# Optimization experiments

Hardware: AMD Instinct MI355X
Metric: run time of the kernel (lower is better)

## Reference

```python
import jax, jax.numpy as jnp
import numpy as np

EPS = 1e-5  # eqx.nn.LayerNorm default


def _layer_norm(x, w, b):
    m = x.mean(-1, keepdims=True)
    v = ((x - m) ** 2).mean(-1, keepdims=True)
    return (x - m) / jnp.sqrt(v + EPS) * w + b


def _s4_block(x, nw, nb, lre, lim, bre, bim, cre, cim, d, lstep, ow, ob, o2w, o2b):
    # x: [L, H]. One SequenceBlock: LayerNorm -> S4 recurrence (lax.scan) -> GELU -> GLU-style gated linear -> residual.
    skip = x
    h = _layer_norm(x, nw, nb)
    Lam = lre + 1j * lim                      # [H, N] complex diagonal state matrix
    step = jnp.exp(lstep)[:, None]            # [H, 1] per-channel timescale
    BL = 1.0 / (1.0 - (step / 2.0) * Lam)     # bilinear discretization
    Abar = BL * (1.0 + (step / 2.0) * Lam)    # [H, N]
    Bbar = BL * step * (bre + 1j * bim)       # [H, N]
    C = cre + 1j * cim                        # [H, N]

    def scan_fn(state, u):                    # state: [H, N] complex, u: [H]
        new = Abar * state + Bbar * u[:, None]
        y = 2.0 * jnp.sum(C * new, axis=-1).real + d * u
        return new, y

    init = jnp.zeros(Abar.shape, Abar.dtype)  # cell.init_state
    _, y = jax.lax.scan(scan_fn, init, h)     # [L, H]
    y = jax.nn.gelu(y)
    y = (y @ ow.T + ob) * jax.nn.sigmoid(y @ o2w.T + o2b)
    return skip + y


def setup_inputs() -> dict:
    key = jax.random.key(0)
    L, IN, OUT, H, N, NL = 2048, 4, 3, 512, 32, 4
    ks = jax.random.split(key, 16)
    return {
        "x": jax.random.normal(ks[0], (L, IN), jnp.float32),
        "enc_w": jax.random.normal(ks[1], (H, IN), jnp.float32) / np.sqrt(IN),
        "enc_b": jnp.zeros((H,), jnp.float32),
        "dec_w": jax.random.normal(ks[2], (OUT, H), jnp.float32) / np.sqrt(H),
        "dec_b": jnp.zeros((OUT,), jnp.float32),
        "norm_w": jnp.ones((NL, H), jnp.float32),
        "norm_b": jnp.zeros((NL, H), jnp.float32),
        "lam_re": -0.5 - jax.random.uniform(ks[3], (NL, H, N), jnp.float32),  # stable (Re < 0)
        "lam_im": np.pi * jax.random.normal(ks[4], (NL, H, N), jnp.float32),
        "b_re": jax.random.normal(ks[5], (NL, H, N), jnp.float32) / np.sqrt(N),
        "b_im": jax.random.normal(ks[6], (NL, H, N), jnp.float32) / np.sqrt(N),
        "c_re": jax.random.normal(ks[7], (NL, H, N), jnp.float32) / np.sqrt(N),
        "c_im": jax.random.normal(ks[8], (NL, H, N), jnp.float32) / np.sqrt(N),
        "d": jax.random.normal(ks[9], (NL, H), jnp.float32),
        "log_step": float(np.log(1e-3)) + float(np.log(1e-1) - np.log(1e-3)) * jax.random.uniform(ks[10], (NL, H), jnp.float32),
        "out_w": jax.random.normal(ks[11], (NL, H, H), jnp.float32) / np.sqrt(H),
        "out_b": jnp.zeros((NL, H), jnp.float32),
        "out2_w": jax.random.normal(ks[12], (NL, H, H), jnp.float32) / np.sqrt(H),
        "out2_b": jnp.zeros((NL, H), jnp.float32),
    }


def reference(x, enc_w, enc_b, dec_w, dec_b, norm_w, norm_b, lam_re, lam_im, b_re, b_im, c_re, c_im, d, log_step, out_w, out_b, out2_w, out2_b):
    h = x @ enc_w.T + enc_b                   # encoder: [L, IN] -> [L, H]
    for i in range(norm_w.shape[0]):          # fixed small n_layers loop
        h = _s4_block(h, norm_w[i], norm_b[i], lam_re[i], lam_im[i], b_re[i], b_im[i],
                      c_re[i], c_im[i], d[i], log_step[i], out_w[i], out_b[i], out2_w[i], out2_b[i])
    return h @ dec_w.T + dec_b                # decoder: [L, H] -> [L, OUT]
```

## Files before the change

kernel.cpp:

```cpp
#include <hip/hip_runtime.h>
#include <hip/hip_bf16.h>
#include <math.h>

#define LSEQ 2048
#define HD   512
#define NST  32
#define LC   32
#define NCHK 64
#define HH   (HD * HD)

typedef __bf16 bf16;
typedef __bf16 bf16x8 __attribute__((ext_vector_type(8)));
typedef float  floatx4 __attribute__((ext_vector_type(4)));

__device__ __forceinline__ float wave_reduce_add(float v) {
#pragma unroll
    for (int m = 32; m; m >>= 1) v += __shfl_xor(v, m, 64);
    return v;
}

__device__ __forceinline__ float gelu_tanh(float x) {
    float z = 0.7978845608028654f * (x + 0.044715f * x * x * x);
    float e = __expf(2.f * z);
    float th = 1.f - 2.f / (e + 1.f);
    return 0.5f * x * (1.f + th);
}

__device__ __forceinline__ void make_ab(float lre, float lim, float step,
                                        float br0, float bi0,
                                        float& ar, float& ai, float& br, float& bi) {
    float s2 = 0.5f * step;
    float dr = 1.f - s2 * lre, di = -s2 * lim;
    float inv = 1.f / (dr * dr + di * di);
    float blr = dr * inv, bli = -di * inv;
    float nr = 1.f + s2 * lre, ni = s2 * lim;
    ar = blr * nr - bli * ni;
    ai = blr * ni + bli * nr;
    float tr = step * br0, ti = step * bi0;
    br = blr * tr - bli * ti;
    bi = blr * ti + bli * tr;
}

__global__ __launch_bounds__(256) void setup_kernel(
    const float* __restrict__ x,   const float* __restrict__ ew,
    const float* __restrict__ eb,
    const float* __restrict__ lre, const float* __restrict__ lim,
    const float* __restrict__ bre, const float* __restrict__ bim,
    const float* __restrict__ cre, const float* __restrict__ cim,
    const float* __restrict__ ls,  const float* __restrict__ ow,
    const float* __restrict__ o2w,
    float* __restrict__ h, bf16* __restrict__ wb,
    float2* __restrict__ cA, float2* __restrict__ cB,
    float2* __restrict__ cC, float2* __restrict__ cAp,
    float* __restrict__ st0)
{
    int bid = blockIdx.x, tid = threadIdx.x;
    if (bid < 256) {
        int tg = bid * 256 + tid;
        int lay = tg >> 14, rem = tg & 16383;
        int ch = rem >> 5, n = rem & 31;
        float step = __expf(ls[lay * HD + ch]);
        float ar, ai, br, bi;
        make_ab(lre[tg], lim[tg], step, bre[tg], bim[tg], ar, ai, br, bi);
        float xr = ar, xi = ai;
#pragma unroll
        for (int q = 0; q < 5; ++q) { float tt = xr * xr - xi * xi; xi = 2.f * xr * xi; xr = tt; }
        int dst = (lay * NST + n) * HD + ch;
        cA[dst]  = make_float2(ar, ai);
        cB[dst]  = make_float2(br, bi);
        cC[dst]  = make_float2(2.f * cre[tg], 2.f * cim[tg]);
        cAp[dst] = make_float2(xr, xi);
    } else if (bid < 768) {
        int i = ((bid - 256) * 256 + tid) * 8;
        float4 a = *(const float4*)(ow + i);
        float4 b = *(const float4*)(ow + i + 4);
        bf16x8 o;
        o[0]=(bf16)a.x; o[1]=(bf16)a.y; o[2]=(bf16)a.z; o[3]=(bf16)a.w;
        o[4]=(bf16)b.x; o[5]=(bf16)b.y; o[6]=(bf16)b.z; o[7]=(bf16)b.w;
        *(bf16x8*)(wb + i) = o;
        a = *(const float4*)(o2w + i);
        b = *(const float4*)(o2w + i + 4);
        o[0]=(bf16)a.x; o[1]=(bf16)a.y; o[2]=(bf16)a.z; o[3]=(bf16)a.w;
        o[4]=(bf16)b.x; o[5]=(bf16)b.y; o[6]=(bf16)b.z; o[7]=(bf16)b.w;
        *(bf16x8*)(wb + 4 * HH + i) = o;
    } else {
        int i = (bid - 768) * 256 + tid;
        int t = i >> 9, c = i & 511;
        float4 xv = *(const float4*)(x + t * 4);
        float4 wv = *(const float4*)(ew + c * 4);
        float acc = eb[c];
        acc = fmaf(xv.x, wv.x, acc); acc = fmaf(xv.y, wv.y, acc);
        acc = fmaf(xv.z, wv.z, acc); acc = fmaf(xv.w, wv.w, acc);
        h[i] = acc;
        float s1 = wave_reduce_add(acc);
        float s2 = wave_reduce_add(acc * acc);
        if ((tid & 63) == 0) {
            atomicAdd(&st0[t * 2],     s1);
            atomicAdd(&st0[t * 2 + 1], s2);
        }
    }
}

__global__ __launch_bounds__(256, 2) void p1_kernel(
    const float* __restrict__ h, const float* __restrict__ st,
    const float2* __restrict__ cA, const float2* __restrict__ cB,
    const float* __restrict__ nw, const float* __restrict__ nb,
    float2* __restrict__ f, int lay) {
    __shared__ float  tile[4 * LC * 16];
    __shared__ float2 sml[128];
    __shared__ float  snw[16], snb[16];
    int tid = threadIdx.x;
    int lane = tid & 63, w = tid >> 6;
    int chl = lane & 15;
    int ch = blockIdx.x * 16 + chl;
    int sub = lane >> 4;
    int chunk = blockIdx.y * 4 + w;
    int t0 = blockIdx.y * 4 * LC;
    const float* ub = h + (size_t)t0 * HD + blockIdx.x * 16;
#pragma unroll
    for (int r = 0; r < 8; ++r) {
        int idx = r * 256 + tid;
        tile[idx] = ub[(idx >> 4) * HD + (idx & 15)];
    }
    if (tid < 128) {
        float s1 = st[(t0 + tid) * 2], s2 = st[(t0 + tid) * 2 + 1];
        float m = s1 * (1.f / HD);
        float var = s2 * (1.f / HD) - m * m;
        sml[tid] = make_float2(m, rsqrtf(var + 1e-5f));
    }
    if (tid < 16) {
        snw[tid] = nw[lay * HD + blockIdx.x * 16 + tid];
        snb[tid] = nb[lay * HD + blockIdx.x * 16 + tid];
    }
    int cbase = (lay * NST + sub * 8) * HD + ch;
    float aR[8], aI[8], bR[8], bI[8];
#pragma unroll
    for (int j = 0; j < 8; ++j) {
        float2 t = cA[cbase + j * HD]; aR[j] = t.x; aI[j] = t.y;
        t = cB[cbase + j * HD];        bR[j] = t.x; bI[j] = t.y;
    }
    float sr[8], si[8];
#pragma unroll
    for (int j = 0; j < 8; ++j) { sr[j] = 0.f; si[j] = 0.f; }
    __syncthreads();
    float wch = snw[chl], bch = snb[chl];
#pragma unroll 4
    for (int t = 0; t < LC; ++t) {
        int row = w * LC + t;
        float2 ms = sml[row];
        float uu = (tile[row * 16 + chl] - ms.x) * ms.y * wch + bch;
#pragma unroll
        for (int j = 0; j < 8; ++j) {
            float nr = fmaf(aR[j], sr[j], fmaf(-aI[j], si[j], bR[j] * uu));
            float ni = fmaf(aI[j], sr[j], fmaf( aR[j], si[j], bI[j] * uu));
            sr[j] = nr; si[j] = ni;
        }
    }
    float2* fp = f + ((size_t)chunk * NST + sub * 8) * HD + ch;
#pragma unroll
    for (int j = 0; j < 8; ++j) fp[j * HD] = make_float2(sr[j], si[j]);
}

__global__ __launch_bounds__(256) void p2_kernel(
    float2* __restrict__ f, const float2* __restrict__ cAp, int lay) {
    int w = threadIdx.x >> 6, lane = threadIdx.x & 63;
    int chain = blockIdx.x * 4 + w;
    int ch = chain & 511, n = chain >> 9;
    float2 ap = cAp[(lay * NST + n) * HD + ch];
    size_t idx = ((size_t)lane * NST + n) * HD + ch;
    float2 v = f[idx];
    float vr = v.x, vi = v.y, wr = ap.x, wi = ap.y;
#pragma unroll
    for (int d = 1; d < 64; d <<= 1) {
        float pvr = __shfl_up(vr, d, 64);
        float pvi = __shfl_up(vi, d, 64);
        float pwr = __shfl_up(wr, d, 64);
        float pwi = __shfl_up(wi, d, 64);
        if (lane >= d) {
            vr += wr * pvr - wi * pvi;
            vi += wr * pvi + wi * pvr;
            float nr = wr * pwr - wi * pwi;
            float ni = wr * pwi + wi * pwr;
            wr = nr; wi = ni;
        }
    }
    f[idx] = make_float2(vr, vi);
}

__global__ __launch_bounds__(256, 2) void p3_kernel(
    const float* __restrict__ h, const float* __restrict__ st,
    const float2* __restrict__ f,
    const float2* __restrict__ cA, const float2* __restrict__ cB,
    const float2* __restrict__ cC, const float* __restrict__ dd,
    const float* __restrict__ nw, const float* __restrict__ nb,
    bf16* __restrict__ g, int lay) {
    __shared__ float  tile[4 * LC * 16];
    __shared__ float2 sml[128];
    __shared__ float  snw[16], snb[16];
    int tid = threadIdx.x;
    int lane = tid & 63, w = tid >> 6;
    int chl = lane & 15;
    int ch = blockIdx.x * 16 + chl;
    int sub = lane >> 4;
    int chunk = blockIdx.y * 4 + w;
    int t0 = blockIdx.y * 4 * LC;
    const float* ub = h + (size_t)t0 * HD + blockIdx.x * 16;
#pragma unroll
    for (int r = 0; r < 8; ++r) {
        int idx = r * 256 + tid;
        tile[idx] = ub[(idx >> 4) * HD + (idx & 15)];
    }
    if (tid < 128) {
        float s1 = st[(t0 + tid) * 2], s2 = st[(t0 + tid) * 2 + 1];
        float m = s1 * (1.f / HD);
        float var = s2 * (1.f / HD) - m * m;
        sml[tid] = make_float2(m, rsqrtf(var + 1e-5f));
    }
    if (tid < 16) {
        snw[tid] = nw[lay * HD + blockIdx.x * 16 + tid];
        snb[tid] = nb[lay * HD + blockIdx.x * 16 + tid];
    }
    int cbase = (lay * NST + sub * 8) * HD + ch;
    float aR[8], aI[8], bR[8], bI[8], cR[8], cI[8];
#pragma unroll
    for (int j = 0; j < 8; ++j) {
        float2 t = cA[cbase + j * HD]; aR[j] = t.x; aI[j] = t.y;
        t = cB[cbase + j * HD];        bR[j] = t.x; bI[j] = t.y;
        t = cC[cbase + j * HD];        cR[j] = t.x; cI[j] = t.y;
    }
    float dch = dd[lay * HD + ch];
    float sr[8], si[8];
    if (chunk > 0) {
        const float2* ip = f + ((size_t)(chunk - 1) * NST + sub * 8) * HD + ch;
#pragma unroll
        for (int j = 0; j < 8; ++j) { float2 v = ip[j * HD]; sr[j] = v.x; si[j] = v.y; }
    } else {
#pragma unroll
        for (int j = 0; j < 8; ++j) { sr[j] = 0.f; si[j] = 0.f; }
    }
    __syncthreads();
    float wch = snw[chl], bch = snb[chl];
    bf16* gp = g + (size_t)chunk * LC * HD + ch;
#pragma unroll 4
    for (int t = 0; t < LC; ++t) {
        int row = w * LC + t;
        float2 ms = sml[row];
        float uu = (tile[row * 16 + chl] - ms.x) * ms.y * wch + bch;
        float p = 0.f;
#pragma unroll
        for (int j = 0; j < 8; ++j) {
            float nr = fmaf(aR[j], sr[j], fmaf(-aI[j], si[j], bR[j] * uu));
            float ni = fmaf(aI[j], sr[j], fmaf( aR[j], si[j], bI[j] * uu));
            sr[j] = nr; si[j] = ni;
            p = fmaf(cR[j], nr, fmaf(-cI[j], ni, p));
        }
        p += __shfl_xor(p, 16);
        p += __shfl_xor(p, 32);
        float y = fmaf(dch, uu, p);
        if (sub == 0) gp[t * HD] = (bf16)gelu_tanh(y);
    }
}

__global__ __launch_bounds__(256) void mm_kernel(
    const bf16* __restrict__ A,
    const bf16* __restrict__ W1,
    const bf16* __restrict__ W2,
    const float* __restrict__ bias1, const float* __restrict__ bias2,
    float* __restrict__ Hio, float* __restrict__ stn) {
    const int w = threadIdx.x >> 6, lane = threadIdx.x & 63;
    const int wm = w >> 1, wn = w & 1;
    const int mBase = blockIdx.y * 64 + wm * 32;
    const int nBase = blockIdx.x * 64 + wn * 32;
    const int lrow = lane & 15, quad = lane >> 4;

    floatx4 acc1[2][2] = {{{0.f,0.f,0.f,0.f},{0.f,0.f,0.f,0.f}},{{0.f,0.f,0.f,0.f},{0.f,0.f,0.f,0.f}}};
    floatx4 acc2[2][2] = {{{0.f,0.f,0.f,0.f},{0.f,0.f,0.f,0.f}},{{0.f,0.f,0.f,0.f},{0.f,0.f,0.f,0.f}}};

    for (int k0 = 0; k0 < HD; k0 += 32) {
        int kk = k0 + quad * 8;
        bf16x8 a0 = *(const bf16x8*)(A + (mBase + lrow) * HD + kk);
        bf16x8 a1 = *(const bf16x8*)(A + (mBase + 16 + lrow) * HD + kk);
        bf16x8 p0 = *(const bf16x8*)(W1 + (nBase + lrow) * HD + kk);
        bf16x8 p1 = *(const bf16x8*)(W1 + (nBase + 16 + lrow) * HD + kk);
        bf16x8 q0 = *(const bf16x8*)(W2 + (nBase + lrow) * HD + kk);
        bf16x8 q1 = *(const bf16x8*)(W2 + (nBase + 16 + lrow) * HD + kk);
        acc1[0][0] = __builtin_amdgcn_mfma_f32_16x16x32_bf16(a0, p0, acc1[0][0], 0, 0, 0);
        acc1[0][1] = __builtin_amdgcn_mfma_f32_16x16x32_bf16(a0, p1, acc1[0][1], 0, 0, 0);
        acc1[1][0] = __builtin_amdgcn_mfma_f32_16x16x32_bf16(a1, p0, acc1[1][0], 0, 0, 0);
        acc1[1][1] = __builtin_amdgcn_mfma_f32_16x16x32_bf16(a1, p1, acc1[1][1], 0, 0, 0);
        acc2[0][0] = __builtin_amdgcn_mfma_f32_16x16x32_bf16(a0, q0, acc2[0][0], 0, 0, 0);
        acc2[0][1] = __builtin_amdgcn_mfma_f32_16x16x32_bf16(a0, q1, acc2[0][1], 0, 0, 0);
        acc2[1][0] = __builtin_amdgcn_mfma_f32_16x16x32_bf16(a1, q0, acc2[1][0], 0, 0, 0);
        acc2[1][1] = __builtin_amdgcn_mfma_f32_16x16x32_bf16(a1, q1, acc2[1][1], 0, 0, 0);
    }

    float hv[2][2][4];
#pragma unroll
    for (int fm = 0; fm < 2; ++fm)
#pragma unroll
        for (int fn = 0; fn < 2; ++fn) {
            int j = nBase + fn * 16 + lrow;
            float bb1 = bias1[j], bb2 = bias2[j];
#pragma unroll
            for (int r = 0; r < 4; ++r) {
                int t = mBase + fm * 16 + quad * 4 + r;
                float z1 = acc1[fm][fn][r] + bb1;
                float z2 = acc2[fm][fn][r] + bb2;
                float nv = Hio[t * HD + j] + z1 / (1.f + __expf(-z2));
                Hio[t * HD + j] = nv;
                hv[fm][fn][r] = nv;
            }
        }
#pragma unroll
    for (int fm = 0; fm < 2; ++fm)
#pragma unroll
        for (int r = 0; r < 4; ++r) {
            int t = mBase + fm * 16 + quad * 4 + r;
            float s1 = hv[fm][0][r] + hv[fm][1][r];
            float s2 = hv[fm][0][r] * hv[fm][0][r] + hv[fm][1][r] * hv[fm][1][r];
#pragma unroll
            for (int m = 1; m < 16; m <<= 1) {
                s1 += __shfl_xor(s1, m);
                s2 += __shfl_xor(s2, m);
            }
            if (lrow == 0) {
                atomicAdd(&stn[t * 2],     s1);
                atomicAdd(&stn[t * 2 + 1], s2);
            }
        }
}

__global__ __launch_bounds__(192) void dec_kernel(
    const float* __restrict__ h, const float* __restrict__ w,
    const float* __restrict__ b, float* __restrict__ out) {
    int j = threadIdx.x >> 6, lane = threadIdx.x & 63;
    int t = blockIdx.x;
    const float* hp = h + t * HD + lane * 8;
    float v[8];
    *(float4*)(v)     = *(const float4*)(hp);
    *(float4*)(v + 4) = *(const float4*)(hp + 4);
    float w8[8];
    *(float4*)(w8)     = *(const float4*)(w + j * HD + lane * 8);
    *(float4*)(w8 + 4) = *(const float4*)(w + j * HD + lane * 8 + 4);
    float s = 0.f;
#pragma unroll
    for (int e = 0; e < 8; ++e) s = fmaf(v[e], w8[e], s);
    s = wave_reduce_add(s);
    if (lane == 0) out[t * 3 + j] = s + b[j];
}

extern "C" void kernel_launch(void* const* d_in, const int* in_sizes, int n_in,
                              void* d_out, int out_size, void* d_ws, size_t ws_size,
                              hipStream_t stream) {
    const float* x   = (const float*)d_in[0];
    const float* ew  = (const float*)d_in[1];
    const float* eb  = (const float*)d_in[2];
    const float* dw  = (const float*)d_in[3];
    const float* db  = (const float*)d_in[4];
    const float* nw  = (const float*)d_in[5];
    const float* nb  = (const float*)d_in[6];
    const float* lre = (const float*)d_in[7];
    const float* lim = (const float*)d_in[8];
    const float* bre = (const float*)d_in[9];
    const float* bim = (const float*)d_in[10];
    const float* cre = (const float*)d_in[11];
    const float* cim = (const float*)d_in[12];
    const float* dd  = (const float*)d_in[13];
    const float* ls  = (const float*)d_in[14];
    const float* ow  = (const float*)d_in[15];
    const float* ob  = (const float*)d_in[16];
    const float* o2w = (const float*)d_in[17];
    const float* o2b = (const float*)d_in[18];
    char* ws = (char*)d_ws;

    float*  h     = (float*)ws;
    float2* f     = (float2*)(ws + (4  << 20));
    bf16*   g     = (bf16*)(ws + (12 << 20));
    bf16*   wb    = (bf16*)(ws + (14 << 20));
    float*  stats = (float*)(ws + (18 << 20));
    float2* cA    = (float2*)(ws + (19 << 20));
    float2* cB    = cA + 4 * NST * HD;
    float2* cC    = cB + 4 * NST * HD;
    float2* cAp   = cC + 4 * NST * HD;

    hipMemsetAsync(stats, 0, 5 * LSEQ * 2 * sizeof(float), stream);
    setup_kernel<<<4864, 256, 0, stream>>>(x, ew, eb, lre, lim, bre, bim,
                                           cre, cim, ls, ow, o2w,
                                           h, wb, cA, cB, cC, cAp, stats);
    for (int lay = 0; lay < 4; ++lay) {
        float* st  = stats + lay * LSEQ * 2;
        float* stn = stats + (lay + 1) * LSEQ * 2;
        p1_kernel<<<dim3(32, 16), 256, 0, stream>>>(h, st, cA, cB, nw, nb, f, lay);
        p2_kernel<<<4096, 256, 0, stream>>>(f, cAp, lay);
        p3_kernel<<<dim3(32, 16), 256, 0, stream>>>(h, st, f, cA, cB, cC, dd, nw, nb, g, lay);
        mm_kernel<<<dim3(8, 32), 256, 0, stream>>>(
            g, wb + lay * HH, wb + 4 * HH + lay * HH,
            ob + lay * HD, o2b + lay * HD, h, stn);
    }
    dec_kernel<<<LSEQ, 192, 0, stream>>>(h, dw, db, (float*)d_out);
}
```

Baseline: 362.9 us.

## Split chunk-carry scan into three passes and halve channels per block

The single-wave Kogge-Stone shuffle scan over 64 chunk carries is replaced by three kernels. The first scans within super-chunks of 8, the second scans super-chunk carries using A^8, and the third applies those carries back to each chunk. The chunked scan kernels now handle 8 channels per block with 4 states per lane instead of 16 channels and 8 states, which doubles the grid and cuts register pressure. In exchange there are two extra kernel launches per layer and more passes over the carry buffer, plus an extra shuffle step in the C·state reduction.

```diff
diff --git a/kernel.cpp b/kernel.cpp
--- a/kernel.cpp
+++ b/kernel.cpp
@@ -7,6 +7,8 @@
 #define NST  32
 #define LC   32
 #define NCHK 64
+#define SUP  8
+#define NSUP 8
 #define HH   (HD * HD)
 
 typedef __bf16 bf16;
@@ -101,26 +103,26 @@
     }
 }
 
-__global__ __launch_bounds__(256, 2) void p1_kernel(
+__global__ __launch_bounds__(256) void p1_kernel(
     const float* __restrict__ h, const float* __restrict__ st,
     const float2* __restrict__ cA, const float2* __restrict__ cB,
     const float* __restrict__ nw, const float* __restrict__ nb,
     float2* __restrict__ f, int lay) {
-    __shared__ float  tile[4 * LC * 16];
+    __shared__ float  tile[4 * LC * 8];
     __shared__ float2 sml[128];
-    __shared__ float  snw[16], snb[16];
+    __shared__ float  snw[8], snb[8];
     int tid = threadIdx.x;
     int lane = tid & 63, w = tid >> 6;
-    int chl = lane & 15;
-    int ch = blockIdx.x * 16 + chl;
-    int sub = lane >> 4;
+    int chl = lane & 7;
+    int ch = blockIdx.x * 8 + chl;
+    int sub = lane >> 3;
     int chunk = blockIdx.y * 4 + w;
     int t0 = blockIdx.y * 4 * LC;
-    const float* ub = h + (size_t)t0 * HD + blockIdx.x * 16;
-#pragma unroll
-    for (int r = 0; r < 8; ++r) {
+    const float* ub = h + (size_t)t0 * HD + blockIdx.x * 8;
+#pragma unroll
+    for (int r = 0; r < 4; ++r) {
         int idx = r * 256 + tid;
-        tile[idx] = ub[(idx >> 4) * HD + (idx & 15)];
+        tile[idx] = ub[(idx >> 3) * HD + (idx & 7)];
     }
     if (tid < 128) {
         float s1 = st[(t0 + tid) * 2], s2 = st[(t0 + tid) * 2 + 1];
@@ -128,87 +130,122 @@
         float var = s2 * (1.f / HD) - m * m;
         sml[tid] = make_float2(m, rsqrtf(var + 1e-5f));
     }
-    if (tid < 16) {
-        snw[tid] = nw[lay * HD + blockIdx.x * 16 + tid];
-        snb[tid] = nb[lay * HD + blockIdx.x * 16 + tid];
-    }
-    int cbase = (lay * NST + sub * 8) * HD + ch;
-    float aR[8], aI[8], bR[8], bI[8];
-#pragma unroll
-    for (int j = 0; j < 8; ++j) {
+    if (tid < 8) {
+        snw[tid] = nw[lay * HD + blockIdx.x * 8 + tid];
+        snb[tid] = nb[lay * HD + blockIdx.x * 8 + tid];
+    }
+    int cbase = (lay * NST + sub * 4) * HD + ch;
+    float aR[4], aI[4], bR[4], bI[4];
+#pragma unroll
+    for (int j = 0; j < 4; ++j) {
         float2 t = cA[cbase + j * HD]; aR[j] = t.x; aI[j] = t.y;
         t = cB[cbase + j * HD];        bR[j] = t.x; bI[j] = t.y;
     }
-    float sr[8], si[8];
-#pragma unroll
-    for (int j = 0; j < 8; ++j) { sr[j] = 0.f; si[j] = 0.f; }
+    float sr[4] = {0,0,0,0}, si[4] = {0,0,0,0};
     __syncthreads();
     float wch = snw[chl], bch = snb[chl];
 #pragma unroll 4
     for (int t = 0; t < LC; ++t) {
         int row = w * LC + t;
         float2 ms = sml[row];
-        float uu = (tile[row * 16 + chl] - ms.x) * ms.y * wch + bch;
-#pragma unroll
-        for (int j = 0; j < 8; ++j) {
+        float uu = (tile[row * 8 + chl] - ms.x) * ms.y * wch + bch;
+#pragma unroll
+        for (int j = 0; j < 4; ++j) {
             float nr = fmaf(aR[j], sr[j], fmaf(-aI[j], si[j], bR[j] * uu));
             float ni = fmaf(aI[j], sr[j], fmaf( aR[j], si[j], bI[j] * uu));
             sr[j] = nr; si[j] = ni;
         }
     }
-    float2* fp = f + ((size_t)chunk * NST + sub * 8) * HD + ch;
-#pragma unroll
-    for (int j = 0; j < 8; ++j) fp[j * HD] = make_float2(sr[j], si[j]);
-}
-
-__global__ __launch_bounds__(256) void p2_kernel(
+    float2* fp = f + ((size_t)chunk * NST + sub * 4) * HD + ch;
+#pragma unroll
+    for (int j = 0; j < 4; ++j) fp[j * HD] = make_float2(sr[j], si[j]);
+}
+
+__global__ __launch_bounds__(256) void p2a_kernel(
     float2* __restrict__ f, const float2* __restrict__ cAp, int lay) {
-    int w = threadIdx.x >> 6, lane = threadIdx.x & 63;
-    int chain = blockIdx.x * 4 + w;
-    int ch = chain & 511, n = chain >> 9;
+    int tg = blockIdx.x * 256 + threadIdx.x;
+    int ch = tg & 511;
+    int ns = tg >> 9;
+    int n = ns & 31, sup = ns >> 5;
     float2 ap = cAp[(lay * NST + n) * HD + ch];
-    size_t idx = ((size_t)lane * NST + n) * HD + ch;
-    float2 v = f[idx];
-    float vr = v.x, vi = v.y, wr = ap.x, wi = ap.y;
-#pragma unroll
-    for (int d = 1; d < 64; d <<= 1) {
-        float pvr = __shfl_up(vr, d, 64);
-        float pvi = __shfl_up(vi, d, 64);
-        float pwr = __shfl_up(wr, d, 64);
-        float pwi = __shfl_up(wi, d, 64);
-        if (lane >= d) {
-            vr += wr * pvr - wi * pvi;
-            vi += wr * pvi + wi * pvr;
-            float nr = wr * pwr - wi * pwi;
-            float ni = wr * pwi + wi * pwr;
-            wr = nr; wi = ni;
-        }
-    }
-    f[idx] = make_float2(vr, vi);
-}
-
-__global__ __launch_bounds__(256, 2) void p3_kernel(
+    float2* fp = f + ((size_t)(sup * SUP) * NST + n) * HD + ch;
+    float sr = 0.f, si = 0.f;
+#pragma unroll
+    for (int j = 0; j < SUP; ++j) {
+        float2 v = fp[(size_t)j * NST * HD];
+        float nr = fmaf(ap.x, sr, fmaf(-ap.y, si, v.x));
+        float ni = fmaf(ap.y, sr, fmaf( ap.x, si, v.y));
+        sr = nr; si = ni;
+        fp[(size_t)j * NST * HD] = make_float2(sr, si);
+    }
+}
+
+__global__ __launch_bounds__(256) void p2b_kernel(
+    float2* __restrict__ f, const float2* __restrict__ cAp, int lay) {
+    int tg = blockIdx.x * 256 + threadIdx.x;
+    int ch = tg & 511, n = tg >> 9;
+    float2 ap = cAp[(lay * NST + n) * HD + ch];
+    float xr = ap.x, xi = ap.y;
+#pragma unroll
+    for (int q = 0; q < 3; ++q) { float tt = xr * xr - xi * xi; xi = 2.f * xr * xi; xr = tt; }
+    float2* fp = f + ((size_t)(SUP - 1) * NST + n) * HD + ch;
+    const size_t stride = (size_t)SUP * NST * HD;
+    float sr = 0.f, si = 0.f;
+#pragma unroll
+    for (int k = 0; k < NSUP; ++k) {
+        float2 v = fp[k * stride];
+        float nr = fmaf(xr, sr, fmaf(-xi, si, v.x));
+        float ni = fmaf(xi, sr, fmaf( xr, si, v.y));
+        sr = nr; si = ni;
+        fp[k * stride] = make_float2(sr, si);
+    }
+}
+
+__global__ __launch_bounds__(256) void p2c_kernel(
+    float2* __restrict__ f, const float2* __restrict__ cAp, int lay) {
+    int tg = blockIdx.x * 256 + threadIdx.x;
+    int ch = tg & 511;
+    int ns = tg >> 9;
+    int n = ns & 31, sup = ns >> 5;
+    if (sup == 0) return;
+    float2 ap = cAp[(lay * NST + n) * HD + ch];
+    float2 S = f[((size_t)(sup * SUP - 1) * NST + n) * HD + ch];
+    float2* fp = f + ((size_t)(sup * SUP) * NST + n) * HD + ch;
+    float wr = ap.x, wi = ap.y;
+#pragma unroll
+    for (int j = 0; j < SUP - 1; ++j) {
+        float2 v = fp[(size_t)j * NST * HD];
+        v.x += wr * S.x - wi * S.y;
+        v.y += wr * S.y + wi * S.x;
+        fp[(size_t)j * NST * HD] = v;
+        float nwr = wr * ap.x - wi * ap.y;
+        float nwi = wr * ap.y + wi * ap.x;
+        wr = nwr; wi = nwi;
+    }
+}
+
+__global__ __launch_bounds__(256) void p3_kernel(
     const float* __restrict__ h, const float* __restrict__ st,
     const float2* __restrict__ f,
     const float2* __restrict__ cA, const float2* __restrict__ cB,
     const float2* __restrict__ cC, const float* __restrict__ dd,
     const float* __restrict__ nw, const float* __restrict__ nb,
     bf16* __restrict__ g, int lay) {
-    __shared__ float  tile[4 * LC * 16];
+    __shared__ float  tile[4 * LC * 8];
     __shared__ float2 sml[128];
-    __shared__ float  snw[16], snb[16];
+    __shared__ float  snw[8], snb[8];
     int tid = threadIdx.x;
     int lane = tid & 63, w = tid >> 6;
-    int chl = lane & 15;
-    int ch = blockIdx.x * 16 + chl;
-    int sub = lane >> 4;
+    int chl = lane & 7;
+    int ch = blockIdx.x * 8 + chl;
+    int sub = lane >> 3;
     int chunk = blockIdx.y * 4 + w;
     int t0 = blockIdx.y * 4 * LC;
-    const float* ub = h + (size_t)t0 * HD + blockIdx.x * 16;
-#pragma unroll
-    for (int r = 0; r < 8; ++r) {
+    const float* ub = h + (size_t)t0 * HD + blockIdx.x * 8;
+#pragma unroll
+    for (int r = 0; r < 4; ++r) {
         int idx = r * 256 + tid;
-        tile[idx] = ub[(idx >> 4) * HD + (idx & 15)];
+        tile[idx] = ub[(idx >> 3) * HD + (idx & 7)];
     }
     if (tid < 128) {
         float s1 = st[(t0 + tid) * 2], s2 = st[(t0 + tid) * 2 + 1];
@@ -216,48 +253,51 @@
         float var = s2 * (1.f / HD) - m * m;
         sml[tid] = make_float2(m, rsqrtf(var + 1e-5f));
     }
-    if (tid < 16) {
-        snw[tid] = nw[lay * HD + blockIdx.x * 16 + tid];
-        snb[tid] = nb[lay * HD + blockIdx.x * 16 + tid];
-    }
-    int cbase = (lay * NST + sub * 8) * HD + ch;
-    float aR[8], aI[8], bR[8], bI[8], cR[8], cI[8];
-#pragma unroll
-    for (int j = 0; j < 8; ++j) {
+    if (tid < 8) {
+        snw[tid] = nw[lay * HD + blockIdx.x * 8 + tid];
+        snb[tid] = nb[lay * HD + blockIdx.x * 8 + tid];
+    }
+    int cbase = (lay * NST + sub * 4) * HD + ch;
+    float aR[4], aI[4], bR[4], bI[4], cR[4], cI[4];
+#pragma unroll
+    for (int j = 0; j < 4; ++j) {
         float2 t = cA[cbase + j * HD]; aR[j] = t.x; aI[j] = t.y;
         t = cB[cbase + j * HD];        bR[j] = t.x; bI[j] = t.y;
         t = cC[cbase + j * HD];        cR[j] = t.x; cI[j] = t.y;
     }
     float dch = dd[lay * HD + ch];
-    float sr[8], si[8];
+    float sr[4], si[4];
     if (chunk > 0) {
-        const float2* ip = f + ((size_t)(chunk - 1) * NST + sub * 8) * HD + ch;
-#pragma unroll
-        for (int j = 0; j < 8; ++j) { float2 v = ip[j * HD]; sr[j] = v.x; si[j] = v.y; }
+        const float2* ip = f + ((size_t)(chunk - 1) * NST + sub * 4) * HD + ch;
+#pragma unroll
+        for (int j = 0; j < 4; ++j) { float2 v = ip[j * HD]; sr[j] = v.x; si[j] = v.y; }
     } else {
 #pragma unroll
-        for (int j = 0; j < 8; ++j) { sr[j] = 0.f; si[j] = 0.f; }
+        for (int j = 0; j < 4; ++j) { sr[j] = 0.f; si[j] = 0.f; }
     }
     __syncthreads();
     float wch = snw[chl], bch = snb[chl];
-    bf16* gp = g + (size_t)chunk * LC * HD + ch;
+    bf16* gp = g + (size_t)t0 * HD + ch;
 #pragma unroll 4
     for (int t = 0; t < LC; ++t) {
         int row = w * LC + t;
         float2 ms = sml[row];
-        float uu = (tile[row * 16 + chl] - ms.x) * ms.y * wch + bch;
-        float p = 0.f;
-#pragma unroll
-        for (int j = 0; j < 8; ++j) {
+        float uu = (tile[row * 8 + chl] - ms.x) * ms.y * wch + bch;
+        float p0 = 0.f, p1 = 0.f;
+#pragma unroll
+        for (int j = 0; j < 4; ++j) {
             float nr = fmaf(aR[j], sr[j], fmaf(-aI[j], si[j], bR[j] * uu));
             float ni = fmaf(aI[j], sr[j], fmaf( aR[j], si[j], bI[j] * uu));
             sr[j] = nr; si[j] = ni;
-            p = fmaf(cR[j], nr, fmaf(-cI[j], ni, p));
+            p0 = fmaf(cR[j], nr, p0);
+            p1 = fmaf(-cI[j], ni, p1);
         }
+        float p = p0 + p1;
+        p += __shfl_xor(p, 8);
         p += __shfl_xor(p, 16);
         p += __shfl_xor(p, 32);
         float y = fmaf(dch, uu, p);
-        if (sub == 0) gp[t * HD] = (bf16)gelu_tanh(y);
+        if (sub == 0) gp[(size_t)row * HD] = (bf16)gelu_tanh(y);
     }
 }
 
@@ -390,9 +430,11 @@
     for (int lay = 0; lay < 4; ++lay) {
         float* st  = stats + lay * LSEQ * 2;
         float* stn = stats + (lay + 1) * LSEQ * 2;
-        p1_kernel<<<dim3(32, 16), 256, 0, stream>>>(h, st, cA, cB, nw, nb, f, lay);
-        p2_kernel<<<4096, 256, 0, stream>>>(f, cAp, lay);
-        p3_kernel<<<dim3(32, 16), 256, 0, stream>>>(h, st, f, cA, cB, cC, dd, nw, nb, g, lay);
+        p1_kernel<<<dim3(64, 16), 256, 0, stream>>>(h, st, cA, cB, nw, nb, f, lay);
+        p2a_kernel<<<512, 256, 0, stream>>>(f, cAp, lay);
+        p2b_kernel<<<64, 256, 0, stream>>>(f, cAp, lay);
+        p2c_kernel<<<512, 256, 0, stream>>>(f, cAp, lay);
+        p3_kernel<<<dim3(64, 16), 256, 0, stream>>>(h, st, f, cA, cB, cC, dd, nw, nb, g, lay);
         mm_kernel<<<dim3(8, 32), 256, 0, stream>>>(
             g, wb + lay * HH, wb + 4 * HH + lay * HH,
             ob + lay * HD, o2b + lay * HD, h, stn);
```

Result: faster. 339.0 us (-6.6%).

## Fuse chunked scan passes into single kernel with decoupled look-back across chunks

Applied to the files above, without the earlier changes.

Replaces the three-kernel chunked scan (local chunk scan, cross-chunk prefix, rescan with output) with one kernel. Block order comes from an atomic ticket, and each block publishes its chunk's local end state with a flag. Later blocks spin on earlier flags and combine the aggregates serially using A^128. Chunks grow from 32 to 128 steps, and each thread now handles 2 states instead of 8, which cuts launches and f-buffer traffic. In exchange it adds spin-wait latency and a serial look-back of up to 15 chunks.

```diff
diff --git a/kernel.cpp b/kernel.cpp
--- a/kernel.cpp
+++ b/kernel.cpp
@@ -5,8 +5,9 @@
 #define LSEQ 2048
 #define HD   512
 #define NST  32
-#define LC   32
-#define NCHK 64
+#define LC   128
+#define NCHK 16
+#define NCG  32
 #define HH   (HD * HD)
 
 typedef __bf16 bf16;
@@ -64,7 +65,7 @@
         make_ab(lre[tg], lim[tg], step, bre[tg], bim[tg], ar, ai, br, bi);
         float xr = ar, xi = ai;
 #pragma unroll
-        for (int q = 0; q < 5; ++q) { float tt = xr * xr - xi * xi; xi = 2.f * xr * xi; xr = tt; }
+        for (int q = 0; q < 7; ++q) { float tt = xr * xr - xi * xi; xi = 2.f * xr * xi; xr = tt; }
         int dst = (lay * NST + n) * HD + ch;
         cA[dst]  = make_float2(ar, ai);
         cB[dst]  = make_float2(br, bi);
@@ -101,163 +102,137 @@
     }
 }
 
-__global__ __launch_bounds__(256, 2) void p1_kernel(
+__global__ __launch_bounds__(256) void scan_kernel(
     const float* __restrict__ h, const float* __restrict__ st,
     const float2* __restrict__ cA, const float2* __restrict__ cB,
+    const float2* __restrict__ cC, const float2* __restrict__ cAp,
+    const float* __restrict__ dd,
     const float* __restrict__ nw, const float* __restrict__ nb,
-    float2* __restrict__ f, int lay) {
-    __shared__ float  tile[4 * LC * 16];
-    __shared__ float2 sml[128];
+    bf16* __restrict__ g, float2* __restrict__ agg,
+    int* __restrict__ flags, int* __restrict__ ticket, int lay)
+{
+    __shared__ float  tile[LC * 16];
+    __shared__ float2 sml[LC];
     __shared__ float  snw[16], snb[16];
-    int tid = threadIdx.x;
-    int lane = tid & 63, w = tid >> 6;
-    int chl = lane & 15;
-    int ch = blockIdx.x * 16 + chl;
-    int sub = lane >> 4;
-    int chunk = blockIdx.y * 4 + w;
-    int t0 = blockIdx.y * 4 * LC;
-    const float* ub = h + (size_t)t0 * HD + blockIdx.x * 16;
+    __shared__ int    vt_s;
+    const int tid = threadIdx.x;
+    if (tid == 0) vt_s = atomicAdd(&ticket[lay], 1);
+    __syncthreads();
+    const int vt = vt_s;
+    const int cg = vt & 31, c = vt >> 5;
+    const int ch0 = cg * 16, t0 = c * LC;
+    const int chl = tid >> 4, sub = tid & 15;
+    const int ch = ch0 + chl, n0 = sub * 2;
+    int* lflags = flags + lay * NCG * NCHK + cg * NCHK;
+
 #pragma unroll
     for (int r = 0; r < 8; ++r) {
         int idx = r * 256 + tid;
-        tile[idx] = ub[(idx >> 4) * HD + (idx & 15)];
-    }
-    if (tid < 128) {
+        tile[idx] = h[(size_t)(t0 + (idx >> 4)) * HD + ch0 + (idx & 15)];
+    }
+    if (tid < LC) {
         float s1 = st[(t0 + tid) * 2], s2 = st[(t0 + tid) * 2 + 1];
         float m = s1 * (1.f / HD);
         float var = s2 * (1.f / HD) - m * m;
         sml[tid] = make_float2(m, rsqrtf(var + 1e-5f));
     }
     if (tid < 16) {
-        snw[tid] = nw[lay * HD + blockIdx.x * 16 + tid];
-        snb[tid] = nb[lay * HD + blockIdx.x * 16 + tid];
-    }
-    int cbase = (lay * NST + sub * 8) * HD + ch;
-    float aR[8], aI[8], bR[8], bI[8];
-#pragma unroll
-    for (int j = 0; j < 8; ++j) {
-        float2 t = cA[cbase + j * HD]; aR[j] = t.x; aI[j] = t.y;
-        t = cB[cbase + j * HD];        bR[j] = t.x; bI[j] = t.y;
-    }
-    float sr[8], si[8];
-#pragma unroll
-    for (int j = 0; j < 8; ++j) { sr[j] = 0.f; si[j] = 0.f; }
+        snw[tid] = nw[lay * HD + ch0 + tid];
+        snb[tid] = nb[lay * HD + ch0 + tid];
+    }
+    float aR[2], aI[2], bR[2], bI[2], cR[2], cI[2], apR[2], apI[2];
+#pragma unroll
+    for (int j = 0; j < 2; ++j) {
+        int ci = (lay * NST + n0 + j) * HD + ch;
+        float2 t = cA[ci];  aR[j] = t.x;  aI[j] = t.y;
+        t = cB[ci];         bR[j] = t.x;  bI[j] = t.y;
+        t = cC[ci];         cR[j] = t.x;  cI[j] = t.y;
+        t = cAp[ci];        apR[j] = t.x; apI[j] = t.y;
+    }
+    float dch = dd[lay * HD + ch];
     __syncthreads();
-    float wch = snw[chl], bch = snb[chl];
+    const float wch = snw[chl], bch = snb[chl];
+
+    float sr[2] = {0.f, 0.f}, si[2] = {0.f, 0.f};
 #pragma unroll 4
     for (int t = 0; t < LC; ++t) {
-        int row = w * LC + t;
-        float2 ms = sml[row];
-        float uu = (tile[row * 16 + chl] - ms.x) * ms.y * wch + bch;
-#pragma unroll
-        for (int j = 0; j < 8; ++j) {
+        float2 ms = sml[t];
+        float uu = (tile[t * 16 + chl] - ms.x) * ms.y * wch + bch;
+#pragma unroll
+        for (int j = 0; j < 2; ++j) {
             float nr = fmaf(aR[j], sr[j], fmaf(-aI[j], si[j], bR[j] * uu));
             float ni = fmaf(aI[j], sr[j], fmaf( aR[j], si[j], bI[j] * uu));
             sr[j] = nr; si[j] = ni;
         }
     }
-    float2* fp = f + ((size_t)chunk * NST + sub * 8) * HD + ch;
-#pragma unroll
-    for (int j = 0; j < 8; ++j) fp[j * HD] = make_float2(sr[j], si[j]);
-}
-
-__global__ __launch_bounds__(256) void p2_kernel(
-    float2* __restrict__ f, const float2* __restrict__ cAp, int lay) {
-    int w = threadIdx.x >> 6, lane = threadIdx.x & 63;
-    int chain = blockIdx.x * 4 + w;
-    int ch = chain & 511, n = chain >> 9;
-    float2 ap = cAp[(lay * NST + n) * HD + ch];
-    size_t idx = ((size_t)lane * NST + n) * HD + ch;
-    float2 v = f[idx];
-    float vr = v.x, vi = v.y, wr = ap.x, wi = ap.y;
-#pragma unroll
-    for (int d = 1; d < 64; d <<= 1) {
-        float pvr = __shfl_up(vr, d, 64);
-        float pvi = __shfl_up(vi, d, 64);
-        float pwr = __shfl_up(wr, d, 64);
-        float pwi = __shfl_up(wi, d, 64);
-        if (lane >= d) {
-            vr += wr * pvr - wi * pvi;
-            vi += wr * pvi + wi * pvr;
-            float nr = wr * pwr - wi * pwi;
-            float ni = wr * pwi + wi * pwr;
-            wr = nr; wi = ni;
-        }
-    }
-    f[idx] = make_float2(vr, vi);
-}
-
-__global__ __launch_bounds__(256, 2) void p3_kernel(
-    const float* __restrict__ h, const float* __restrict__ st,
-    const float2* __restrict__ f,
-    const float2* __restrict__ cA, const float2* __restrict__ cB,
-    const float2* __restrict__ cC, const float* __restrict__ dd,
-    const float* __restrict__ nw, const float* __restrict__ nb,
-    bf16* __restrict__ g, int lay) {
-    __shared__ float  tile[4 * LC * 16];
-    __shared__ float2 sml[128];
-    __shared__ float  snw[16], snb[16];
-    int tid = threadIdx.x;
-    int lane = tid & 63, w = tid >> 6;
-    int chl = lane & 15;
-    int ch = blockIdx.x * 16 + chl;
-    int sub = lane >> 4;
-    int chunk = blockIdx.y * 4 + w;
-    int t0 = blockIdx.y * 4 * LC;
-    const float* ub = h + (size_t)t0 * HD + blockIdx.x * 16;
-#pragma unroll
-    for (int r = 0; r < 8; ++r) {
-        int idx = r * 256 + tid;
-        tile[idx] = ub[(idx >> 4) * HD + (idx & 15)];
-    }
-    if (tid < 128) {
-        float s1 = st[(t0 + tid) * 2], s2 = st[(t0 + tid) * 2 + 1];
-        float m = s1 * (1.f / HD);
-        float var = s2 * (1.f / HD) - m * m;
-        sml[tid] = make_float2(m, rsqrtf(var + 1e-5f));
-    }
-    if (tid < 16) {
-        snw[tid] = nw[lay * HD + blockIdx.x * 16 + tid];
-        snb[tid] = nb[lay * HD + blockIdx.x * 16 + tid];
-    }
-    int cbase = (lay * NST + sub * 8) * HD + ch;
-    float aR[8], aI[8], bR[8], bI[8], cR[8], cI[8];
-#pragma unroll
-    for (int j = 0; j < 8; ++j) {
-        float2 t = cA[cbase + j * HD]; aR[j] = t.x; aI[j] = t.y;
-        t = cB[cbase + j * HD];        bR[j] = t.x; bI[j] = t.y;
-        t = cC[cbase + j * HD];        cR[j] = t.x; cI[j] = t.y;
-    }
-    float dch = dd[lay * HD + ch];
-    float sr[8], si[8];
-    if (chunk > 0) {
-        const float2* ip = f + ((size_t)(chunk - 1) * NST + sub * 8) * HD + ch;
-#pragma unroll
-        for (int j = 0; j < 8; ++j) { float2 v = ip[j * HD]; sr[j] = v.x; si[j] = v.y; }
-    } else {
-#pragma unroll
-        for (int j = 0; j < 8; ++j) { sr[j] = 0.f; si[j] = 0.f; }
-    }
+    {
+        size_t a = ((size_t)(cg * NCHK + c) * 512) + chl * 32 + n0;
+        agg[a]     = make_float2(sr[0], si[0]);
+        agg[a + 1] = make_float2(sr[1], si[1]);
+    }
+    __threadfence();
     __syncthreads();
-    float wch = snw[chl], bch = snb[chl];
-    bf16* gp = g + (size_t)chunk * LC * HD + ch;
+    if (tid == 0) atomicExch(&lflags[c], 1);
+
+    float Sr[2] = {0.f, 0.f}, Si[2] = {0.f, 0.f};
+    if (c > 0) {
+        if (tid < c) {
+            while (atomicAdd(&lflags[tid], 0) == 0) __builtin_amdgcn_s_sleep(2);
+        }
+        __syncthreads();
+        __threadfence();
+        float2 B0[8], B1[8];
+#pragma unroll
+        for (int i = 0; i < 8; ++i) if (i < c) {
+            size_t a = ((size_t)(cg * NCHK + i) * 512) + chl * 32 + n0;
+            B0[i] = agg[a]; B1[i] = agg[a + 1];
+        }
+#pragma unroll
+        for (int i = 0; i < 8; ++i) if (i < c) {
+            float nr = fmaf(apR[0], Sr[0], fmaf(-apI[0], Si[0], B0[i].x));
+            float ni = fmaf(apI[0], Sr[0], fmaf( apR[0], Si[0], B0[i].y));
+            Sr[0] = nr; Si[0] = ni;
+            nr = fmaf(apR[1], Sr[1], fmaf(-apI[1], Si[1], B1[i].x));
+            ni = fmaf(apI[1], Sr[1], fmaf( apR[1], Si[1], B1[i].y));
+            Sr[1] = nr; Si[1] = ni;
+        }
+#pragma unroll
+        for (int i = 8; i < 15; ++i) if (i < c) {
+            size_t a = ((size_t)(cg * NCHK + i) * 512) + chl * 32 + n0;
+            B0[i - 8] = agg[a]; B1[i - 8] = agg[a + 1];
+        }
+#pragma unroll
+        for (int i = 8; i < 15; ++i) if (i < c) {
+            float nr = fmaf(apR[0], Sr[0], fmaf(-apI[0], Si[0], B0[i - 8].x));
+            float ni = fmaf(apI[0], Sr[0], fmaf( apR[0], Si[0], B0[i - 8].y));
+            Sr[0] = nr; Si[0] = ni;
+            nr = fmaf(apR[1], Sr[1], fmaf(-apI[1], Si[1], B1[i - 8].x));
+            ni = fmaf(apI[1], Sr[1], fmaf( apR[1], Si[1], B1[i - 8].y));
+            Sr[1] = nr; Si[1] = ni;
+        }
+    }
+
+    sr[0] = Sr[0]; si[0] = Si[0]; sr[1] = Sr[1]; si[1] = Si[1];
+    bf16* gp = g + (size_t)t0 * HD + ch;
 #pragma unroll 4
     for (int t = 0; t < LC; ++t) {
-        int row = w * LC + t;
-        float2 ms = sml[row];
-        float uu = (tile[row * 16 + chl] - ms.x) * ms.y * wch + bch;
-        float p = 0.f;
-#pragma unroll
-        for (int j = 0; j < 8; ++j) {
+        float2 ms = sml[t];
+        float uu = (tile[t * 16 + chl] - ms.x) * ms.y * wch + bch;
+        float p0 = 0.f, p1 = 0.f;
+#pragma unroll
+        for (int j = 0; j < 2; ++j) {
             float nr = fmaf(aR[j], sr[j], fmaf(-aI[j], si[j], bR[j] * uu));
             float ni = fmaf(aI[j], sr[j], fmaf( aR[j], si[j], bI[j] * uu));
             sr[j] = nr; si[j] = ni;
-            p = fmaf(cR[j], nr, fmaf(-cI[j], ni, p));
-        }
-        p += __shfl_xor(p, 16);
-        p += __shfl_xor(p, 32);
-        float y = fmaf(dch, uu, p);
-        if (sub == 0) gp[t * HD] = (bf16)gelu_tanh(y);
+            p0 = fmaf(cR[j], nr, p0);
+            p1 = fmaf(-cI[j], ni, p1);
+        }
+        float p = p0 + p1;
+        p += __shfl_xor(p, 1);
+        p += __shfl_xor(p, 2);
+        p += __shfl_xor(p, 4);
+        p += __shfl_xor(p, 8);
+        if (sub == 0) gp[(size_t)t * HD] = (bf16)gelu_tanh(fmaf(dch, uu, p));
     }
 }
 
@@ -373,26 +348,27 @@
     const float* o2b = (const float*)d_in[18];
     char* ws = (char*)d_ws;
 
-    float*  h     = (float*)ws;
-    float2* f     = (float2*)(ws + (4  << 20));
-    bf16*   g     = (bf16*)(ws + (12 << 20));
-    bf16*   wb    = (bf16*)(ws + (14 << 20));
-    float*  stats = (float*)(ws + (18 << 20));
-    float2* cA    = (float2*)(ws + (19 << 20));
-    float2* cB    = cA + 4 * NST * HD;
-    float2* cC    = cB + 4 * NST * HD;
-    float2* cAp   = cC + 4 * NST * HD;
-
-    hipMemsetAsync(stats, 0, 5 * LSEQ * 2 * sizeof(float), stream);
+    float*  h      = (float*)ws;
+    float2* agg    = (float2*)(ws + (4 << 20));
+    bf16*   g      = (bf16*)(ws + (6 << 20));
+    bf16*   wb     = (bf16*)(ws + (8 << 20));
+    float*  stats  = (float*)(ws + (12 << 20));
+    int*    flags  = (int*)(ws + (12 << 20) + (256 << 10));
+    int*    ticket = (int*)(ws + (12 << 20) + (384 << 10));
+    float2* cA     = (float2*)(ws + (13 << 20));
+    float2* cB     = cA + 4 * NST * HD;
+    float2* cC     = cB + 4 * NST * HD;
+    float2* cAp    = cC + 4 * NST * HD;
+
+    hipMemsetAsync(ws + (12 << 20), 0, 512 << 10, stream);
     setup_kernel<<<4864, 256, 0, stream>>>(x, ew, eb, lre, lim, bre, bim,
                                            cre, cim, ls, ow, o2w,
                                            h, wb, cA, cB, cC, cAp, stats);
     for (int lay = 0; lay < 4; ++lay) {
         float* st  = stats + lay * LSEQ * 2;
         float* stn = stats + (lay + 1) * LSEQ * 2;
-        p1_kernel<<<dim3(32, 16), 256, 0, stream>>>(h, st, cA, cB, nw, nb, f, lay);
-        p2_kernel<<<4096, 256, 0, stream>>>(f, cAp, lay);
-        p3_kernel<<<dim3(32, 16), 256, 0, stream>>>(h, st, f, cA, cB, cC, dd, nw, nb, g, lay);
+        scan_kernel<<<NCG * NCHK, 256, 0, stream>>>(
+            h, st, cA, cB, cC, cAp, dd, nw, nb, g, agg, flags, ticket, lay);
         mm_kernel<<<dim3(8, 32), 256, 0, stream>>>(
             g, wb + lay * HH, wb + 4 * HH + lay * HH,
             ob + lay * HD, o2b + lay * HD, h, stn);
```

After: 737.4 us. 103% more time.
